# Kernel tuning notes

Hardware: AMD Instinct MI355X
Metric: run time of the kernel (lower is better)

The kernel has to match this reference:

```python
import jax, jax.numpy as jnp
import numpy as np

C = 256
NUM_HEADS = 4
GROUPS = 8
EPS = 1e-5


def setup_inputs() -> dict:
    key = jax.random.key(0)
    ks = jax.random.split(key, 8)
    N, H, W = 4, 64, 64
    x = jax.random.normal(ks[0], (N, C, H, W), dtype=jnp.float32)
    mask = jnp.ones((N, 1, H, W), dtype=jnp.float32)
    norm_w = jax.random.normal(ks[1], (C,), dtype=jnp.float32) * 0.02 + 1.0
    norm_b = jax.random.normal(ks[2], (C,), dtype=jnp.float32) * 0.02
    qkv_w = jax.random.normal(ks[3], (3 * C, C), dtype=jnp.float32) * (1.0 / np.sqrt(C))
    qkv_b = jax.random.normal(ks[4], (3 * C,), dtype=jnp.float32) * 0.02
    proj_w = jax.random.normal(ks[5], (C, C), dtype=jnp.float32) * (1.0 / np.sqrt(C))
    proj_b = jax.random.normal(ks[6], (C,), dtype=jnp.float32) * 0.02
    return {"x": x, "mask": mask, "norm_w": norm_w, "norm_b": norm_b,
            "qkv_w": qkv_w, "qkv_b": qkv_b, "proj_w": proj_w, "proj_b": proj_b}


def _group_norm(x, w, b):
    # x: [N, C, H, W]; normalize within GROUPS groups over (C//G, H, W)
    N, Cc, H, W = x.shape
    xg = x.reshape(N, GROUPS, Cc // GROUPS, H, W)
    mean = xg.mean(axis=(2, 3, 4), keepdims=True)
    var = xg.var(axis=(2, 3, 4), keepdims=True)
    xg = (xg - mean) * jax.lax.rsqrt(var + EPS)
    x = xg.reshape(N, Cc, H, W)
    return x * w[None, :, None, None] + b[None, :, None, None]


def reference(x, mask, norm_w, norm_b, qkv_w, qkv_b, proj_w, proj_b):
    N, Cc, H, W = x.shape
    h = NUM_HEADS
    hd = Cc // h  # head dim
    x_norm = _group_norm(x, norm_w, norm_b)
    # 1x1 conv == channel matmul: [N, 3C, H, W]
    qkv = jnp.einsum('nchw,oc->nohw', x_norm, qkv_w) + qkv_b[None, :, None, None]
    q, k, v = jnp.split(qkv, 3, axis=1)
    # n (h c) y x -> n h (y x) c
    def to_heads(t):
        return t.reshape(N, h, hd, H * W).transpose(0, 1, 3, 2)
    q, k, v = to_heads(q), to_heads(k), to_heads(v)
    scale = hd ** (-0.5)
    scores = jnp.einsum('nhic,nhjc->nhij', q, k) * scale  # [N,h,HW,HW]
    probs = jax.nn.softmax(scores, axis=-1)
    out = jnp.einsum('nhij,nhjc->nhic', probs, v)  # [N,h,HW,hd]
    # n h (y x) c -> n (h c) y x
    out = out.transpose(0, 1, 3, 2).reshape(N, Cc, H, W)
    out = jnp.einsum('nchw,oc->nohw', out, proj_w) + proj_b[None, :, None, None]
    y = (x + out) * mask[:, :1, :, :]  # broadcast over C (== repeat)
    return (y, mask)
```

## Files before the change

kernel.cpp:

```cpp
#include <hip/hip_runtime.h>

#define HW 4096
#define EPSV 1e-5f
#define SCL (0.125f * 1.44269504088896341f)

typedef unsigned short u16;
typedef unsigned int u32;
typedef __attribute__((ext_vector_type(8))) short short8;
typedef __attribute__((ext_vector_type(4))) short short4v;
typedef __attribute__((ext_vector_type(4))) float f32x4;

#define MFMA_K32(a, b, c) __builtin_amdgcn_mfma_f32_16x16x32_bf16((a), (b), (c), 0, 0, 0)
#if __has_builtin(__builtin_amdgcn_mfma_f32_16x16x16bf16_1k)
#define MFMA_K16(a, b, c) __builtin_amdgcn_mfma_f32_16x16x16bf16_1k((a), (b), (c), 0, 0, 0)
#elif __has_builtin(__builtin_amdgcn_mfma_f32_16x16x16_bf16)
#define MFMA_K16(a, b, c) __builtin_amdgcn_mfma_f32_16x16x16_bf16((a), (b), (c), 0, 0, 0)
#else
#define MFMA_K16(a, b, c) (c)
#endif

#define GLDS(g, l) __builtin_amdgcn_global_load_lds( \
    (const __attribute__((address_space(1))) u16*)(g), \
    (__attribute__((address_space(3))) u16*)(l), 16, 0, 0)

__device__ __forceinline__ u16 f2b(float f) {
    u32 u = __float_as_uint(f);
    u32 r = (u + 0x7FFFu + ((u >> 16) & 1u)) >> 16;
    return (u16)r;
}

__global__ __launch_bounds__(256) void gn_partial(const float* __restrict__ x, float* __restrict__ ps) {
    int bid = blockIdx.x;
    const float4* base = (const float4*)x + (size_t)bid * 2048;
    int t = threadIdx.x;
    float s = 0.f, sq = 0.f;
    for (int i = t; i < 2048; i += 256) {
        float4 v = base[i];
        s += v.x + v.y + v.z + v.w;
        sq += v.x * v.x + v.y * v.y + v.z * v.z + v.w * v.w;
    }
    __shared__ float rs[256], rq[256];
    rs[t] = s; rq[t] = sq;
    __syncthreads();
    for (int o = 128; o > 0; o >>= 1) {
        if (t < o) { rs[t] += rs[t + o]; rq[t] += rq[t + o]; }
        __syncthreads();
    }
    if (t == 0) { ps[2 * bid] = rs[0]; ps[2 * bid + 1] = rq[0]; }
}

__global__ __launch_bounds__(64) void gn_final(const float* __restrict__ ps, float* __restrict__ stats) {
    int t = threadIdx.x;
    if (t < 32) {
        float s = 0.f, sq = 0.f;
        for (int i = 0; i < 16; i++) {
            s += ps[2 * (t * 16 + i)];
            sq += ps[2 * (t * 16 + i) + 1];
        }
        float mean = s * (1.f / 131072.f);
        float var = sq * (1.f / 131072.f) - mean * mean;
        stats[t] = mean;
        stats[32 + t] = rsqrtf(var + EPSV);
    }
}

__global__ __launch_bounds__(256) void wconv(const float* __restrict__ src, u16* __restrict__ dst, int nscaled) {
    int idx = blockIdx.x * 256 + threadIdx.x;
    int row = idx >> 6;
    float sc = (row < nscaled) ? SCL : 1.0f;
    float4 v = *((const float4*)src + idx);
    u32 lo = (u32)f2b(v.x * sc) | ((u32)f2b(v.y * sc) << 16);
    u32 hi = (u32)f2b(v.z * sc) | ((u32)f2b(v.w * sc) << 16);
    uint2 o; o.x = lo; o.y = hi;
    *(uint2*)(dst + (size_t)idx * 4) = o;
}

__global__ __launch_bounds__(256) void gn_apply_t(const float* __restrict__ x, const float* __restrict__ w,
                                                  const float* __restrict__ b, const float* __restrict__ stats,
                                                  u16* __restrict__ xt) {
    __shared__ u16 Tt[64][72];
    int t = threadIdx.x;
    int p0 = blockIdx.x * 64;
    int c0 = blockIdx.y * 64;
    int n = blockIdx.z;
    int pc = (t & 15) * 4;
#pragma unroll
    for (int jj = 0; jj < 4; jj++) {
        int r = (t >> 4) + jj * 16;
        int c = c0 + r;
        int grp = n * 8 + (c >> 5);
        float mean = stats[grp], rstd = stats[32 + grp];
        float a = rstd * w[c];
        float bb = b[c] - mean * a;
        float4 v = *(const float4*)(x + ((size_t)n * 256 + c) * HW + p0 + pc);
        Tt[pc + 0][r] = f2b(v.x * a + bb);
        Tt[pc + 1][r] = f2b(v.y * a + bb);
        Tt[pc + 2][r] = f2b(v.z * a + bb);
        Tt[pc + 3][r] = f2b(v.w * a + bb);
    }
    __syncthreads();
    int p = t >> 2, ck = t & 3;
    short8 s0 = *(const short8*)&Tt[p][ck * 16];
    short8 s1 = *(const short8*)&Tt[p][ck * 16 + 8];
    u16* dst = xt + ((size_t)n * HW + p0 + p) * 256 + c0 + ck * 16;
    *(short8*)dst = s0;
    *(short8*)(dst + 8) = s1;
}

__global__ __launch_bounds__(256) void qkv_mfma(const u16* __restrict__ xt, const u16* __restrict__ Wb,
                                                const float* __restrict__ bq, u16* __restrict__ Qw,
                                                u16* __restrict__ Kw, u16* __restrict__ Vw) {
    __shared__ u16 Xs[64 * 256];
    int t = threadIdx.x;
    int w = t >> 6, lane = t & 63;
    int col = lane & 15, quad = lane >> 4;
    int p0 = blockIdx.x * 64;
    int o0 = blockIdx.y * 64;
    int n = blockIdx.z;

#pragma unroll
    for (int j = 0; j < 8; j++) {
        int rl = j * 2 + (lane >> 5);
        int row = w * 16 + rl;
        int slot = (lane & 31) ^ (rl & 7);
        GLDS(xt + ((size_t)n * HW + p0 + row) * 256 + slot * 8, Xs + (w * 16 + j * 2) * 256);
    }

    const u16* wrow = Wb + (size_t)(o0 + w * 16 + col) * 256 + quad * 8;
    short8 A[8];
#pragma unroll
    for (int ks = 0; ks < 8; ks++) A[ks] = *(const short8*)(wrow + ks * 32);

    __syncthreads();

    f32x4 C[4];
#pragma unroll
    for (int pb = 0; pb < 4; pb++) C[pb] = (f32x4){0.f, 0.f, 0.f, 0.f};
    int c7 = col & 7;
#pragma unroll
    for (int pb = 0; pb < 4; pb++) {
        const u16* xr = Xs + (pb * 16 + col) * 256;
#pragma unroll
        for (int ks = 0; ks < 8; ks++) {
            int slot = (ks * 4 + quad) ^ c7;
            short8 Bf = *(const short8*)(xr + slot * 8);
            C[pb] = MFMA_K32(A[ks], Bf, C[pb]);
        }
    }

    int type = o0 >> 8;
    int h = (o0 >> 6) & 3;
    int nh = n * 4 + h;
    float sc = (type == 0) ? SCL : 1.0f;
    if (type == 2) {
#pragma unroll
        for (int rg = 0; rg < 4; rg++) {
            int d = w * 16 + quad * 4 + rg;
            float bias = bq[o0 + d];
            u16* vb = Vw + ((size_t)nh * 64 + d) * HW + p0 + col;
#pragma unroll
            for (int pb = 0; pb < 4; pb++)
                vb[pb * 16] = f2b(C[pb][rg] + bias);
        }
    } else {
        u16* dst = (type == 0 ? Qw : Kw) + ((size_t)nh * HW + p0 + col) * 64 + w * 16 + quad * 4;
        float b0 = sc * bq[o0 + w * 16 + quad * 4 + 0];
        float b1 = sc * bq[o0 + w * 16 + quad * 4 + 1];
        float b2 = sc * bq[o0 + w * 16 + quad * 4 + 2];
        float b3 = sc * bq[o0 + w * 16 + quad * 4 + 3];
#pragma unroll
        for (int pb = 0; pb < 4; pb++) {
            uint2 o;
            o.x = (u32)f2b(C[pb][0] + b0) | ((u32)f2b(C[pb][1] + b1) << 16);
            o.y = (u32)f2b(C[pb][2] + b2) | ((u32)f2b(C[pb][3] + b3) << 16);
            *(uint2*)(dst + (size_t)(pb * 16) * 64) = o;
        }
    }
}

__global__ __launch_bounds__(256) void flash_mfma(const u16* __restrict__ Qw, const u16* __restrict__ Kw,
                                                  const u16* __restrict__ Vw, u16* __restrict__ attnT) {
    __shared__ u16 Ks[2][128 * 64];
    __shared__ u16 Vts[2][64 * 128];
    int t = threadIdx.x;
    int w = t >> 6, lane = t & 63;
    int col = lane & 15, quad = lane >> 4;
    int q0 = blockIdx.x * 128;
    int nh = blockIdx.y;

    const u16* qp = Qw + ((size_t)nh * HW + q0 + w * 32 + col) * 64 + quad * 8;
    short8 qa0 = *(const short8*)qp;
    short8 qa1 = *(const short8*)(qp + 32);
    short8 qc0 = *(const short8*)(qp + 1024);
    short8 qc1 = *(const short8*)(qp + 1024 + 32);

    f32x4 OaA[4], OaB[4];
#pragma unroll
    for (int db = 0; db < 4; db++) {
        OaA[db] = (f32x4){0.f, 0.f, 0.f, 0.f};
        OaB[db] = (f32x4){0.f, 0.f, 0.f, 0.f};
    }
    float lA = 0.f, lB = 0.f;

    const u16* kbase = Kw + (size_t)nh * HW * 64;
    const u16* vbase = Vw + (size_t)nh * 64 * HW;
    int lrK = lane >> 3;
    int ccK = lane & 7;
    size_t kSrc = (size_t)(w * 8 + lrK) * 64 + (ccK ^ lrK) * 8;
    int rvV = lane >> 4;
    int cvV = lane & 15;

#define STAGE(jt_, b_) do { \
        int j0_ = (jt_) * 128; \
        _Pragma("unroll") \
        for (int s_ = 0; s_ < 4; s_++) \
            GLDS(kbase + (size_t)j0_ * 64 + kSrc + (size_t)(s_ * 32) * 64, &Ks[b_][(w * 8 + s_ * 32) * 64]); \
        _Pragma("unroll") \
        for (int m_ = 0; m_ < 4; m_++) { \
            int d_ = w * 16 + m_ * 4 + rvV; \
            GLDS(vbase + (size_t)d_ * HW + j0_ + ((cvV ^ (d_ & 7)) * 8), &Vts[b_][(w * 16 + m_ * 4) * 128]); \
        } \
    } while (0)

    STAGE(0, 0);
    __syncthreads();

    int c7 = col & 7;
    for (int jt = 0; jt < 32; jt++) {
        int cur = jt & 1;
        if (jt < 31) STAGE(jt + 1, cur ^ 1);
        const u16* KsC = Ks[cur];
        const u16* VtC = Vts[cur];

        f32x4 sA[8], sB[8];
#pragma unroll
        for (int jb = 0; jb < 8; jb++) {
            const u16* kr = KsC + (jb * 16 + col) * 64;
            short8 ka0 = *(const short8*)(kr + ((quad ^ c7) * 8));
            short8 ka1 = *(const short8*)(kr + (((quad + 4) ^ c7) * 8));
            f32x4 a = (f32x4){0.f, 0.f, 0.f, 0.f};
            a = MFMA_K32(ka0, qa0, a);
            a = MFMA_K32(ka1, qa1, a);
            sA[jb] = a;
            f32x4 b = (f32x4){0.f, 0.f, 0.f, 0.f};
            b = MFMA_K32(ka0, qc0, b);
            b = MFMA_K32(ka1, qc1, b);
            sB[jb] = b;
        }

        short4v ptA[8], ptB[8];
        float lpA = 0.f, lpB = 0.f;
#pragma unroll
        for (int jb = 0; jb < 8; jb++) {
#pragma unroll
            for (int rg = 0; rg < 4; rg++) {
                float pa = __builtin_amdgcn_exp2f(sA[jb][rg]);
                float pb = __builtin_amdgcn_exp2f(sB[jb][rg]);
                lpA += pa; lpB += pb;
                ptA[jb][rg] = (short)(__float_as_uint(pa) >> 16);
                ptB[jb][rg] = (short)(__float_as_uint(pb) >> 16);
            }
        }
        lA += lpA;
        lB += lpB;

#pragma unroll
        for (int db = 0; db < 4; db++) {
            const u16* vr = VtC + (db * 16 + col) * 128;
#pragma unroll
            for (int jb = 0; jb < 8; jb++) {
                int ch = jb * 2 + (quad >> 1);
                short4v va = *(const short4v*)(vr + ((ch ^ c7) * 8) + (quad & 1) * 4);
                OaA[db] = MFMA_K16(va, ptA[jb], OaA[db]);
                OaB[db] = MFMA_K16(va, ptB[jb], OaB[db]);
            }
        }
        __syncthreads();
    }
#undef STAGE

    lA += __shfl_xor(lA, 16);
    lB += __shfl_xor(lB, 16);
    lA += __shfl_xor(lA, 32);
    lB += __shfl_xor(lB, 32);

    float rlA = 1.0f / lA, rlB = 1.0f / lB;
    u16* abA = attnT + ((size_t)(nh >> 2) * HW + q0 + w * 32 + col) * 256 + (nh & 3) * 64 + quad * 4;
    u16* abB = abA + 16 * 256;
#pragma unroll
    for (int db = 0; db < 4; db++) {
        uint2 oA, oB;
        oA.x = (u32)f2b(OaA[db][0] * rlA) | ((u32)f2b(OaA[db][1] * rlA) << 16);
        oA.y = (u32)f2b(OaA[db][2] * rlA) | ((u32)f2b(OaA[db][3] * rlA) << 16);
        oB.x = (u32)f2b(OaB[db][0] * rlB) | ((u32)f2b(OaB[db][1] * rlB) << 16);
        oB.y = (u32)f2b(OaB[db][2] * rlB) | ((u32)f2b(OaB[db][3] * rlB) << 16);
        *(uint2*)(abA + db * 16) = oA;
        *(uint2*)(abB + db * 16) = oB;
    }
}

__global__ __launch_bounds__(256) void proj_mfma(const u16* __restrict__ attnT, const u16* __restrict__ Wpb,
                                                 const float* __restrict__ bp, const float* __restrict__ x,
                                                 const float* __restrict__ mask, float* __restrict__ out) {
    __shared__ u16 Xs[64 * 256];
    int t = threadIdx.x;
    int w = t >> 6, lane = t & 63;
    int col = lane & 15, quad = lane >> 4;
    int p0 = blockIdx.x * 64;
    int o0 = blockIdx.y * 64;
    int n = blockIdx.z;

#pragma unroll
    for (int j = 0; j < 8; j++) {
        int rl = j * 2 + (lane >> 5);
        int row = w * 16 + rl;
        int slot = (lane & 31) ^ (rl & 7);
        GLDS(attnT + ((size_t)n * HW + p0 + row) * 256 + slot * 8, Xs + (w * 16 + j * 2) * 256);
    }

    const u16* wrow = Wpb + (size_t)(o0 + w * 16 + col) * 256 + quad * 8;
    short8 A[8];
#pragma unroll
    for (int ks = 0; ks < 8; ks++) A[ks] = *(const short8*)(wrow + ks * 32);

    __syncthreads();

    f32x4 C[4];
#pragma unroll
    for (int pb = 0; pb < 4; pb++) C[pb] = (f32x4){0.f, 0.f, 0.f, 0.f};
    int c7 = col & 7;
#pragma unroll
    for (int pb = 0; pb < 4; pb++) {
        const u16* xr = Xs + (pb * 16 + col) * 256;
#pragma unroll
        for (int ks = 0; ks < 8; ks++) {
            int slot = (ks * 4 + quad) ^ c7;
            short8 Bf = *(const short8*)(xr + slot * 8);
            C[pb] = MFMA_K32(A[ks], Bf, C[pb]);
        }
    }

#pragma unroll
    for (int rg = 0; rg < 4; rg++) {
        int o = o0 + w * 16 + quad * 4 + rg;
        float bias = bp[o];
        const float* xb = x + ((size_t)n * 256 + o) * HW + p0 + col;
        float* ob = out + ((size_t)n * 256 + o) * HW + p0 + col;
        const float* mb = mask + (size_t)n * HW + p0 + col;
#pragma unroll
        for (int pb = 0; pb < 4; pb++) {
            float mv = mb[pb * 16];
            ob[pb * 16] = (xb[pb * 16] + C[pb][rg] + bias) * mv;
        }
    }
}

__global__ __launch_bounds__(256) void mask_copy(const float* __restrict__ mask, float* __restrict__ out) {
    int i = blockIdx.x * 256 + threadIdx.x;
    out[i] = mask[i];
}

extern "C" void kernel_launch(void* const* d_in, const int* in_sizes, int n_in,
                              void* d_out, int out_size, void* d_ws, size_t ws_size,
                              hipStream_t stream) {
    const float* x = (const float*)d_in[0];
    const float* mask = (const float*)d_in[1];
    const float* norm_w = (const float*)d_in[2];
    const float* norm_b = (const float*)d_in[3];
    const float* qkv_w = (const float*)d_in[4];
    const float* qkv_b = (const float*)d_in[5];
    const float* proj_w = (const float*)d_in[6];
    const float* proj_b = (const float*)d_in[7];
    float* out = (float*)d_out;

    float* ws = (float*)d_ws;
    float* stats = ws;
    float* pstats = ws + 64;
    u16* xt = (u16*)(ws + 2048);
    u16* Qw = xt + 4194304;
    u16* Kw = Qw + 4194304;
    u16* Vw = Kw + 4194304;
    u16* attnT = Vw + 4194304;
    u16* Wqb = attnT + 4194304;
    u16* Wpb = Wqb + 196608;

    gn_partial<<<512, 256, 0, stream>>>(x, pstats);
    gn_final<<<1, 64, 0, stream>>>(pstats, stats);
    wconv<<<192, 256, 0, stream>>>(qkv_w, Wqb, 256);
    wconv<<<64, 256, 0, stream>>>(proj_w, Wpb, 0);
    gn_apply_t<<<dim3(64, 4, 4), 256, 0, stream>>>(x, norm_w, norm_b, stats, xt);
    qkv_mfma<<<dim3(64, 12, 4), 256, 0, stream>>>(xt, Wqb, qkv_b, Qw, Kw, Vw);
    flash_mfma<<<dim3(32, 16), 256, 0, stream>>>(Qw, Kw, Vw, attnT);
    proj_mfma<<<dim3(64, 4, 4), 256, 0, stream>>>(attnT, Wpb, proj_b, x, mask, out);
    mask_copy<<<64, 256, 0, stream>>>(mask, out + 4194304);
}
```

Before: 218.6 us.

## Switch flash attention to 32x32x16 bf16 MFMA tiles with new LDS swizzle

Rewrites the flash attention inner loop to use 32x32x16 bf16 MFMA instructions for both QK^T and PV instead of 16x16x32 and 16x16x16. Each wave now handles a 32-query tile with 16-wide accumulators, and the K/V LDS swizzle is changed to match the new read pattern and avoid bank conflicts. The intent is to cut the number of MFMA issues and LDS reads per FLOP. In exchange it uses larger accumulator registers, and it silently produces zeros if the builtin is missing.

```diff
diff --git a/kernel.cpp b/kernel.cpp
--- a/kernel.cpp
+++ b/kernel.cpp
@@ -9,14 +9,14 @@
 typedef __attribute__((ext_vector_type(8))) short short8;
 typedef __attribute__((ext_vector_type(4))) short short4v;
 typedef __attribute__((ext_vector_type(4))) float f32x4;
+typedef __attribute__((ext_vector_type(16))) float f32x16;
+typedef __attribute__((ext_vector_type(4))) int int4v;
 
 #define MFMA_K32(a, b, c) __builtin_amdgcn_mfma_f32_16x16x32_bf16((a), (b), (c), 0, 0, 0)
-#if __has_builtin(__builtin_amdgcn_mfma_f32_16x16x16bf16_1k)
-#define MFMA_K16(a, b, c) __builtin_amdgcn_mfma_f32_16x16x16bf16_1k((a), (b), (c), 0, 0, 0)
-#elif __has_builtin(__builtin_amdgcn_mfma_f32_16x16x16_bf16)
-#define MFMA_K16(a, b, c) __builtin_amdgcn_mfma_f32_16x16x16_bf16((a), (b), (c), 0, 0, 0)
+#if __has_builtin(__builtin_amdgcn_mfma_f32_32x32x16_bf16)
+#define MFMA32(a, b, c) __builtin_amdgcn_mfma_f32_32x32x16_bf16((a), (b), (c), 0, 0, 0)
 #else
-#define MFMA_K16(a, b, c) (c)
+#define MFMA32(a, b, c) (c)
 #endif
 
 #define GLDS(g, l) __builtin_amdgcn_global_load_lds( \
@@ -184,118 +184,115 @@
     __shared__ u16 Vts[2][64 * 128];
     int t = threadIdx.x;
     int w = t >> 6, lane = t & 63;
-    int col = lane & 15, quad = lane >> 4;
+    int l31 = lane & 31, h = lane >> 5;
     int q0 = blockIdx.x * 128;
     int nh = blockIdx.y;
-
-    const u16* qp = Qw + ((size_t)nh * HW + q0 + w * 32 + col) * 64 + quad * 8;
-    short8 qa0 = *(const short8*)qp;
-    short8 qa1 = *(const short8*)(qp + 32);
-    short8 qc0 = *(const short8*)(qp + 1024);
-    short8 qc1 = *(const short8*)(qp + 1024 + 32);
-
-    f32x4 OaA[4], OaB[4];
-#pragma unroll
-    for (int db = 0; db < 4; db++) {
-        OaA[db] = (f32x4){0.f, 0.f, 0.f, 0.f};
-        OaB[db] = (f32x4){0.f, 0.f, 0.f, 0.f};
-    }
-    float lA = 0.f, lB = 0.f;
+    int key = (l31 & 7) ^ ((l31 >> 3) & 3);
+
+    const u16* qp = Qw + ((size_t)nh * HW + q0 + w * 32 + l31) * 64 + h * 8;
+    short8 Qb[4];
+#pragma unroll
+    for (int c = 0; c < 4; c++) Qb[c] = *(const short8*)(qp + c * 16);
+
+    f32x16 Oc0 = (f32x16)(0.0f), Oc1 = (f32x16)(0.0f);
+    float lsum = 0.f;
 
     const u16* kbase = Kw + (size_t)nh * HW * 64;
     const u16* vbase = Vw + (size_t)nh * 64 * HW;
-    int lrK = lane >> 3;
-    int ccK = lane & 7;
-    size_t kSrc = (size_t)(w * 8 + lrK) * 64 + (ccK ^ lrK) * 8;
-    int rvV = lane >> 4;
-    int cvV = lane & 15;
+    int lrK = lane >> 3, ccK = lane & 7;
+    size_t kSrcOff = (size_t)lrK * 64 + (((ccK ^ lrK ^ w) & 7) * 8);
+    int rvV = lane >> 4, cvV = lane & 15;
 
 #define STAGE(jt_, b_) do { \
         int j0_ = (jt_) * 128; \
         _Pragma("unroll") \
         for (int s_ = 0; s_ < 4; s_++) \
-            GLDS(kbase + (size_t)j0_ * 64 + kSrc + (size_t)(s_ * 32) * 64, &Ks[b_][(w * 8 + s_ * 32) * 64]); \
+            GLDS(kbase + (size_t)(j0_ + w * 8 + s_ * 32) * 64 + kSrcOff, &Ks[b_][(w * 8 + s_ * 32) * 64]); \
         _Pragma("unroll") \
         for (int m_ = 0; m_ < 4; m_++) { \
             int d_ = w * 16 + m_ * 4 + rvV; \
-            GLDS(vbase + (size_t)d_ * HW + j0_ + ((cvV ^ (d_ & 7)) * 8), &Vts[b_][(w * 16 + m_ * 4) * 128]); \
+            int vk_ = (d_ & 7) ^ ((d_ >> 3) & 3); \
+            GLDS(vbase + (size_t)d_ * HW + j0_ + ((cvV ^ vk_) * 8), &Vts[b_][(w * 16 + m_ * 4) * 128]); \
         } \
     } while (0)
 
     STAGE(0, 0);
     __syncthreads();
 
-    int c7 = col & 7;
     for (int jt = 0; jt < 32; jt++) {
         int cur = jt & 1;
         if (jt < 31) STAGE(jt + 1, cur ^ 1);
         const u16* KsC = Ks[cur];
         const u16* VtC = Vts[cur];
-
-        f32x4 sA[8], sB[8];
-#pragma unroll
-        for (int jb = 0; jb < 8; jb++) {
-            const u16* kr = KsC + (jb * 16 + col) * 64;
-            short8 ka0 = *(const short8*)(kr + ((quad ^ c7) * 8));
-            short8 ka1 = *(const short8*)(kr + (((quad + 4) ^ c7) * 8));
-            f32x4 a = (f32x4){0.f, 0.f, 0.f, 0.f};
-            a = MFMA_K32(ka0, qa0, a);
-            a = MFMA_K32(ka1, qa1, a);
-            sA[jb] = a;
-            f32x4 b = (f32x4){0.f, 0.f, 0.f, 0.f};
-            b = MFMA_K32(ka0, qc0, b);
-            b = MFMA_K32(ka1, qc1, b);
-            sB[jb] = b;
-        }
-
-        short4v ptA[8], ptB[8];
-        float lpA = 0.f, lpB = 0.f;
-#pragma unroll
-        for (int jb = 0; jb < 8; jb++) {
-#pragma unroll
-            for (int rg = 0; rg < 4; rg++) {
-                float pa = __builtin_amdgcn_exp2f(sA[jb][rg]);
-                float pb = __builtin_amdgcn_exp2f(sB[jb][rg]);
-                lpA += pa; lpB += pb;
-                ptA[jb][rg] = (short)(__float_as_uint(pa) >> 16);
-                ptB[jb][rg] = (short)(__float_as_uint(pb) >> 16);
+        const u16* vr0 = VtC + l31 * 128 + 4 * h;
+        const u16* vr1 = vr0 + 32 * 128;
+
+#pragma unroll
+        for (int st = 0; st < 4; st++) {
+            const u16* kr = KsC + (st * 32 + l31) * 64;
+            f32x16 c = (f32x16)(0.0f);
+#pragma unroll
+            for (int kc = 0; kc < 4; kc++) {
+                short8 ka = *(const short8*)(kr + (((kc * 2 + h) ^ key) * 8));
+                c = MFMA32(ka, Qb[kc], c);
             }
-        }
-        lA += lpA;
-        lB += lpB;
-
-#pragma unroll
-        for (int db = 0; db < 4; db++) {
-            const u16* vr = VtC + (db * 16 + col) * 128;
-#pragma unroll
-            for (int jb = 0; jb < 8; jb++) {
-                int ch = jb * 2 + (quad >> 1);
-                short4v va = *(const short4v*)(vr + ((ch ^ c7) * 8) + (quad & 1) * 4);
-                OaA[db] = MFMA_K16(va, ptA[jb], OaA[db]);
-                OaB[db] = MFMA_K16(va, ptB[jb], OaB[db]);
+            union { u32 u[4]; short8 s; } b0, b1;
+            float lp = 0.f;
+#pragma unroll
+            for (int r = 0; r < 8; r += 2) {
+                float p0 = __builtin_amdgcn_exp2f(c[r]);
+                float p1 = __builtin_amdgcn_exp2f(c[r + 1]);
+                lp += p0 + p1;
+                b0.u[r >> 1] = (__float_as_uint(p0) >> 16) | (__float_as_uint(p1) & 0xFFFF0000u);
             }
+#pragma unroll
+            for (int r = 8; r < 16; r += 2) {
+                float p0 = __builtin_amdgcn_exp2f(c[r]);
+                float p1 = __builtin_amdgcn_exp2f(c[r + 1]);
+                lp += p0 + p1;
+                b1.u[(r - 8) >> 1] = (__float_as_uint(p0) >> 16) | (__float_as_uint(p1) & 0xFFFF0000u);
+            }
+            lsum += lp;
+#pragma unroll
+            for (int hf = 0; hf < 2; hf++) {
+                int pv = 2 * st + hf;
+                int s1 = ((2 * pv) ^ key) * 8;
+                int s2 = ((2 * pv + 1) ^ key) * 8;
+                short4v a00 = *(const short4v*)(vr0 + s1);
+                short4v a01 = *(const short4v*)(vr0 + s2);
+                short8 va0 = __builtin_shufflevector(a00, a01, 0, 1, 2, 3, 4, 5, 6, 7);
+                short4v a10 = *(const short4v*)(vr1 + s1);
+                short4v a11 = *(const short4v*)(vr1 + s2);
+                short8 va1 = __builtin_shufflevector(a10, a11, 0, 1, 2, 3, 4, 5, 6, 7);
+                if (hf == 0) {
+                    Oc0 = MFMA32(va0, b0.s, Oc0);
+                    Oc1 = MFMA32(va1, b0.s, Oc1);
+                } else {
+                    Oc0 = MFMA32(va0, b1.s, Oc0);
+                    Oc1 = MFMA32(va1, b1.s, Oc1);
+                }
+            }
         }
         __syncthreads();
     }
 #undef STAGE
 
-    lA += __shfl_xor(lA, 16);
-    lB += __shfl_xor(lB, 16);
-    lA += __shfl_xor(lA, 32);
-    lB += __shfl_xor(lB, 32);
-
-    float rlA = 1.0f / lA, rlB = 1.0f / lB;
-    u16* abA = attnT + ((size_t)(nh >> 2) * HW + q0 + w * 32 + col) * 256 + (nh & 3) * 64 + quad * 4;
-    u16* abB = abA + 16 * 256;
-#pragma unroll
-    for (int db = 0; db < 4; db++) {
-        uint2 oA, oB;
-        oA.x = (u32)f2b(OaA[db][0] * rlA) | ((u32)f2b(OaA[db][1] * rlA) << 16);
-        oA.y = (u32)f2b(OaA[db][2] * rlA) | ((u32)f2b(OaA[db][3] * rlA) << 16);
-        oB.x = (u32)f2b(OaB[db][0] * rlB) | ((u32)f2b(OaB[db][1] * rlB) << 16);
-        oB.y = (u32)f2b(OaB[db][2] * rlB) | ((u32)f2b(OaB[db][3] * rlB) << 16);
-        *(uint2*)(abA + db * 16) = oA;
-        *(uint2*)(abB + db * 16) = oB;
+    lsum += __shfl_xor(lsum, 32);
+    float rl = 1.0f / lsum;
+
+    u16* ab = attnT + ((size_t)(nh >> 2) * HW + q0 + w * 32 + l31) * 256 + (nh & 3) * 64 + 4 * h;
+#pragma unroll
+    for (int dt = 0; dt < 2; dt++) {
+#pragma unroll
+        for (int g = 0; g < 4; g++) {
+            float v0, v1, v2, v3;
+            if (dt == 0) { v0 = Oc0[4*g]; v1 = Oc0[4*g+1]; v2 = Oc0[4*g+2]; v3 = Oc0[4*g+3]; }
+            else         { v0 = Oc1[4*g]; v1 = Oc1[4*g+1]; v2 = Oc1[4*g+2]; v3 = Oc1[4*g+3]; }
+            uint2 o;
+            o.x = (u32)f2b(v0 * rl) | ((u32)f2b(v1 * rl) << 16);
+            o.y = (u32)f2b(v2 * rl) | ((u32)f2b(v3 * rl) << 16);
+            *(uint2*)(ab + dt * 32 + g * 8) = o;
+        }
     }
 }
 
```

Result: no change. 220.9 us (+1.0%).
